# Performance work log

Hardware: AMD Instinct MI355X
Metric: run time of the kernel (lower is better)

The kernel has to match this reference:

```python
import jax, jax.numpy as jnp
import numpy as np

B = 16384          # batch_size / n_samples
SRC = 200          # source_num
C = 10             # category_size
I = SRC * C        # input_size = 2000
EPS = 1e-10


def setup_inputs() -> dict:
    key = jax.random.key(0)
    ks = jax.random.split(key, 8)
    # forward data
    x = jax.random.uniform(ks[0], (B, I), dtype=jnp.float32)
    mask = jax.random.uniform(ks[1], (B, I), dtype=jnp.float32)
    y_target = jax.random.uniform(ks[2], (B, C), dtype=jnp.float32)
    # learned parameters (xavier-uniform style init)
    def xavier(k, shape):
        fan_in, fan_out = shape[0], shape[1]
        limit = float(np.sqrt(2.0)) * float(np.sqrt(6.0 / (fan_in + fan_out)))
        return jax.random.uniform(k, shape, dtype=jnp.float32, minval=-limit, maxval=limit)
    W_reconstr = xavier(ks[3], (C, I))
    b_reconstr = xavier(ks[4], (1, I))
    W_yc = xavier(ks[5], (I, C))
    b_yc = xavier(ks[6], (1, C))
    return {"x": x, "mask": mask, "y_target": y_target,
            "W_reconstr": W_reconstr, "b_reconstr": b_reconstr,
            "W_yc": W_yc, "b_yc": b_yc}


def reference(x, mask, y_target, W_reconstr, b_reconstr, W_yc, b_yc):
    # ---- decoder (collapsed): constant_y[i] is a batch of identical one-hot
    # rows at category i, so y @ W_reconstr + b == W_reconstr[i] + b for all
    # batch elements. Stack over all i -> logits [C, I].
    logits = W_reconstr + b_reconstr                      # [C, I]
    e = jnp.exp(logits).reshape(C, SRC, C)                # per-source blocks
    # block-diagonal matmul == segmented sum over each source's C entries
    p = (e / e.sum(axis=-1, keepdims=True)).reshape(C, I)  # [C, I]
    logp = jnp.log(EPS + p)                               # [C, I]
    # -mean_j(mask * x * log p_i) per category i -> [B, C]
    reconstr_x = -(x * mask) @ logp.T / I

    # ---- encoder
    y_classifier = jax.nn.softmax(x @ W_yc + b_yc, axis=1)  # [B, C]

    # ---- losses
    loss_w_l1 = jnp.sum(jnp.abs(W_yc))
    loss_classifier_y_x = jnp.mean(jnp.sum(y_classifier * reconstr_x, axis=1))
    loss_y_kl = jnp.mean(jnp.sum(
        y_classifier * (jnp.log(EPS + y_classifier) - jnp.log(EPS + y_target)),
        axis=1))
    loss = (loss_classifier_y_x + 1e-4 * loss_y_kl
            + 0.005 / SRC / C / C * loss_w_l1)
    return (y_classifier, loss)
```

## Files before the change

### kernel.cpp

```cpp
#include <hip/hip_runtime.h>
#include <hip/hip_bf16.h>

#define B_SZ 16384
#define SRCN 200
#define CAT  10
#define IN   2000
#define QCOL 500
#define QPAD 512
#define NCHQ 8
#define TQB  10240
#define LDS_BUF0 20480
#define EPSF 1e-10f

typedef float f32x4 __attribute__((ext_vector_type(4)));
typedef _Float16 half2v __attribute__((ext_vector_type(2)));

#if __has_builtin(__builtin_amdgcn_fdot2)
__device__ __forceinline__ float fdot2(half2v a, half2v b, float c) {
    return __builtin_amdgcn_fdot2(a, b, c, false);
}
#else
__device__ __forceinline__ float fdot2(half2v a, half2v b, float c) {
    return c + (float)a[0] * (float)b[0] + (float)a[1] * (float)b[1];
}
#endif

__device__ __forceinline__ half2v pkrtz(float a, float b) {
#if __has_builtin(__builtin_amdgcn_cvt_pkrtz)
    union { __fp16 __attribute__((ext_vector_type(2))) i; half2v o; } v;
    v.i = __builtin_amdgcn_cvt_pkrtz(a, b);
    return v.o;
#else
    half2v r; r[0] = (_Float16)a; r[1] = (_Float16)b; return r;
#endif
}

__device__ __forceinline__ half2v as_h2(unsigned u) {
    union { unsigned u; half2v h; } v; v.u = u; return v.h;
}

__device__ __forceinline__ short f2h(float f) {
    union { _Float16 h; short s; } v; v.h = (_Float16)f; return v.s;
}

__device__ __forceinline__ void gload16(const void* g, void* l) {
    __builtin_amdgcn_global_load_lds(
        (const __attribute__((address_space(1))) void*)g,
        (__attribute__((address_space(3))) void*)l,
        16, 0, 0);
}

__global__ void prep_kernel(const float* __restrict__ W_rec,
                            const float* __restrict__ b_rec,
                            const float* __restrict__ W_yc,
                            short* __restrict__ lp4,
                            short* __restrict__ wy4,
                            double* __restrict__ acc) {
    if (blockIdx.x == gridDim.x - 1) {
        float p = 0.f;
        for (int i = threadIdx.x; i < IN * CAT; i += blockDim.x) p += fabsf(W_yc[i]);
        __shared__ float red[4];
        for (int o = 32; o; o >>= 1) p += __shfl_down(p, o, 64);
        if ((threadIdx.x & 63) == 0) red[threadIdx.x >> 6] = p;
        __syncthreads();
        if (threadIdx.x == 0) {
            acc[0] = 0.0; acc[1] = 0.0;
            acc[2] = (double)(red[0] + red[1] + red[2] + red[3]);
        }
        return;
    }
    int idx = blockIdx.x * blockDim.x + threadIdx.x;
    int q   = idx / (CAT * QPAD);
    int rem = idx % (CAT * QPAD);
    int n   = rem >> 9;
    int kk  = rem & 511;
    short wv = 0, lv = 0;
    if (kk < QCOL) {
        int k = q * QCOL + kk;
        wv = f2h(W_yc[k * CAT + n]);
        int base = (k / CAT) * CAT;
        float lg[CAT];
        float m = -1e30f;
        #pragma unroll
        for (int i = 0; i < CAT; i++) {
            lg[i] = W_rec[n * IN + base + i] + b_rec[base + i];
            m = fmaxf(m, lg[i]);
        }
        float s = 0.f;
        #pragma unroll
        for (int i = 0; i < CAT; i++) s += expf(lg[i] - m);
        float myl = W_rec[n * IN + k] + b_rec[k];
        float pp = expf(myl - m) / s;
        lv = f2h(logf(EPSF + pp));
    }
    lp4[idx] = lv;
    wy4[idx] = wv;
}

__global__ __launch_bounds__(512, 3) void main_kernel(
        const float* __restrict__ x, const float* __restrict__ mask,
        const short* __restrict__ lp4, const short* __restrict__ wy4,
        float* __restrict__ part) {
    __shared__ __attribute__((aligned(16))) char lds[LDS_BUF0 + 8 * 4096];

    const int tid = threadIdx.x;
    {
        const int q = blockIdx.x & 3;
        const uint4* s1 = (const uint4*)(lp4 + q * (CAT * QPAD));
        const uint4* s2 = (const uint4*)(wy4 + q * (CAT * QPAD));
        uint4* d1 = (uint4*)lds;
        uint4* d2 = (uint4*)(lds + TQB);
        #pragma unroll
        for (int i = 0; i < 2; ++i) {
            int j = i * 512 + tid;
            if (j < 640) { d1[j] = s1[j]; d2[j] = s2[j]; }
        }
    }
    __syncthreads();

    const int l  = tid & 63;
    const int w  = tid >> 6;
    const int g  = l >> 4;
    const int li = l & 15;
    const int rt = blockIdx.x >> 2;
    const int q  = blockIdx.x & 3;
    const int row = rt * 32 + w * 4 + g;

    const float* xrow = x + (size_t)row * IN;
    const float* mrow = mask + (size_t)row * IN;
    const int colb = q * QCOL + li * 4;
    char* buf = lds + LDS_BUF0 + w * 4096;

    float pR[CAT], pW[CAT];
    #pragma unroll
    for (int c = 0; c < CAT; ++c) { pR[c] = 0.f; pW[c] = 0.f; }

    auto stage = [&](int cc) {
        int col = colb + cc * 64;
        if (col > IN - 4) col = IN - 4;
        char* slot = buf + (cc & 1) * 2048;
        gload16(xrow + col, slot);
        gload16(mrow + col, slot + 1024);
    };

    auto compute = [&](int cc) {
        char* slot = buf + (cc & 1) * 2048;
        const int myo = g * 256 + li * 16;
        f32x4 xv = *(const f32x4*)(slot + myo);
        f32x4 mv = *(const f32x4*)(slot + 1024 + myo);
        half2v ax0 = pkrtz(xv[0], xv[1]);
        half2v ax1 = pkrtz(xv[2], xv[3]);
        half2v am0 = pkrtz(xv[0] * mv[0], xv[1] * mv[1]);
        half2v am1 = pkrtz(xv[2] * mv[2], xv[3] * mv[3]);
        const int tb = cc * 128 + li * 8;
        #pragma unroll
        for (int c = 0; c < CAT; ++c) {
            const uint2 lpv = *(const uint2*)(lds + c * 1024 + tb);
            const uint2 wyv = *(const uint2*)(lds + TQB + c * 1024 + tb);
            pR[c] = fdot2(am0, as_h2(lpv.x), pR[c]);
            pR[c] = fdot2(am1, as_h2(lpv.y), pR[c]);
            pW[c] = fdot2(ax0, as_h2(wyv.x), pW[c]);
            pW[c] = fdot2(ax1, as_h2(wyv.y), pW[c]);
        }
    };

    stage(0);
    stage(1);
    #pragma unroll
    for (int cc = 0; cc < NCHQ; ++cc) {
        if (cc < NCHQ - 1) { asm volatile("s_waitcnt vmcnt(2)" ::: "memory"); }
        else               { asm volatile("s_waitcnt vmcnt(0)" ::: "memory"); }
        compute(cc);
        asm volatile("s_waitcnt lgkmcnt(0)" ::: "memory");
        if (cc + 2 < NCHQ) stage(cc + 2);
    }

    #pragma unroll
    for (int c = 0; c < CAT; ++c) {
        #pragma unroll
        for (int o = 1; o < 16; o <<= 1) {
            pR[c] += __shfl_xor(pR[c], o, 64);
            pW[c] += __shfl_xor(pW[c], o, 64);
        }
    }
    if (li == 0) {
        float* pp = part + ((size_t)row * 4 + q) * 20;
        #pragma unroll
        for (int c = 0; c < CAT; ++c) { pp[c] = pR[c]; pp[10 + c] = pW[c]; }
    }
}

__global__ void combine_kernel(const float* __restrict__ part,
                               const float* __restrict__ y_target,
                               const float* __restrict__ b_yc,
                               float* __restrict__ out,
                               double* __restrict__ acc) {
    const int row = blockIdx.x * 256 + threadIdx.x;
    const float* pp = part + (size_t)row * 80;
    float pR[CAT], pW[CAT];
    #pragma unroll
    for (int c = 0; c < CAT; ++c) {
        pR[c] = pp[c] + pp[20 + c] + pp[40 + c] + pp[60 + c];
        pW[c] = pp[10 + c] + pp[30 + c] + pp[50 + c] + pp[70 + c] + b_yc[c];
    }
    float mx = -1e30f;
    #pragma unroll
    for (int c = 0; c < CAT; ++c) mx = fmaxf(mx, pW[c]);
    float y[CAT], s = 0.f;
    #pragma unroll
    for (int c = 0; c < CAT; ++c) { y[c] = __expf(pW[c] - mx); s += y[c]; }
    const float is = 1.f / s;
    float cls = 0.f, kl = 0.f;
    float* op = out + (size_t)row * CAT;
    #pragma unroll
    for (int c = 0; c < CAT; ++c) {
        y[c] *= is;
        op[c] = y[c];
        cls += y[c] * (-pR[c] * (1.f / IN));
        const float yt = y_target[(size_t)row * CAT + c];
        kl += y[c] * (__logf(EPSF + y[c]) - __logf(EPSF + yt));
    }
    #pragma unroll
    for (int o = 32; o; o >>= 1) {
        cls += __shfl_down(cls, o, 64);
        kl  += __shfl_down(kl, o, 64);
    }
    __shared__ float rc[4], rk[4];
    if ((threadIdx.x & 63) == 0) {
        rc[threadIdx.x >> 6] = cls; rk[threadIdx.x >> 6] = kl;
    }
    __syncthreads();
    if (threadIdx.x == 0) {
        atomicAdd(&acc[0], (double)(rc[0] + rc[1] + rc[2] + rc[3]));
        atomicAdd(&acc[1], (double)(rk[0] + rk[1] + rk[2] + rk[3]));
    }
}

__global__ void final_kernel(const double* __restrict__ acc,
                             float* __restrict__ out) {
    if (threadIdx.x == 0) {
        double loss = acc[0] / (double)B_SZ
                    + 1e-4 * (acc[1] / (double)B_SZ)
                    + (0.005 / (double)SRCN / (double)CAT / (double)CAT) * acc[2];
        out[(size_t)B_SZ * CAT] = (float)loss;
    }
}

extern "C" void kernel_launch(void* const* d_in, const int* in_sizes, int n_in,
                              void* d_out, int out_size, void* d_ws, size_t ws_size,
                              hipStream_t stream) {
    const float* x        = (const float*)d_in[0];
    const float* mask     = (const float*)d_in[1];
    const float* y_target = (const float*)d_in[2];
    const float* W_rec    = (const float*)d_in[3];
    const float* b_rec    = (const float*)d_in[4];
    const float* W_yc     = (const float*)d_in[5];
    const float* b_yc     = (const float*)d_in[6];
    float* out  = (float*)d_out;
    double* acc = (double*)d_ws;
    short* lp4  = (short*)((char*)d_ws + 256);
    short* wy4  = lp4 + 4 * CAT * QPAD;
    float* part = (float*)((char*)d_ws + 256 + 2 * 40960);

    prep_kernel<<<81, 256, 0, stream>>>(W_rec, b_rec, W_yc, lp4, wy4, acc);
    main_kernel<<<2048, 512, 0, stream>>>(x, mask, lp4, wy4, part);
    combine_kernel<<<64, 256, 0, stream>>>(part, y_target, b_yc, out, acc);
    final_kernel<<<1, 64, 0, stream>>>(acc, out);
}
```

Before: 79.79 us.

## Replace LDS-staged double-buffered loads with direct register loads of all chunks

The main kernel stops staging x and mask chunks through LDS with global_load_lds and manual waitcnt double buffering. Each thread now issues all eight float4 loads of x and mask into registers up front, then computes. Blocks shrink from 512 to 256 threads, covering 16 rows instead of 32, and the grid doubles to keep total work the same. This exposes more memory-level parallelism per thread and drops the LDS round trip, at the cost of higher register pressure and smaller blocks that each re-copy the lookup tables into LDS.

```diff
diff --git a/kernel.cpp b/kernel.cpp
--- a/kernel.cpp
+++ b/kernel.cpp
@@ -7,12 +7,9 @@
 #define IN   2000
 #define QCOL 500
 #define QPAD 512
-#define NCHQ 8
 #define TQB  10240
-#define LDS_BUF0 20480
 #define EPSF 1e-10f
 
-typedef float f32x4 __attribute__((ext_vector_type(4)));
 typedef _Float16 half2v __attribute__((ext_vector_type(2)));
 
 #if __has_builtin(__builtin_amdgcn_fdot2)
@@ -41,13 +38,6 @@
 
 __device__ __forceinline__ short f2h(float f) {
     union { _Float16 h; short s; } v; v.h = (_Float16)f; return v.s;
-}
-
-__device__ __forceinline__ void gload16(const void* g, void* l) {
-    __builtin_amdgcn_global_load_lds(
-        (const __attribute__((address_space(1))) void*)g,
-        (__attribute__((address_space(3))) void*)l,
-        16, 0, 0);
 }
 
 __global__ void prep_kernel(const float* __restrict__ W_rec,
@@ -97,61 +87,59 @@
     wy4[idx] = wv;
 }
 
-__global__ __launch_bounds__(512, 3) void main_kernel(
+__global__ __launch_bounds__(256, 4) void main_kernel(
         const float* __restrict__ x, const float* __restrict__ mask,
         const short* __restrict__ lp4, const short* __restrict__ wy4,
         float* __restrict__ part) {
-    __shared__ __attribute__((aligned(16))) char lds[LDS_BUF0 + 8 * 4096];
-
-    const int tid = threadIdx.x;
+    __shared__ __attribute__((aligned(16))) char lds[2 * TQB];
+
+    const int q = blockIdx.x & 3;
     {
-        const int q = blockIdx.x & 3;
         const uint4* s1 = (const uint4*)(lp4 + q * (CAT * QPAD));
         const uint4* s2 = (const uint4*)(wy4 + q * (CAT * QPAD));
         uint4* d1 = (uint4*)lds;
         uint4* d2 = (uint4*)(lds + TQB);
         #pragma unroll
-        for (int i = 0; i < 2; ++i) {
-            int j = i * 512 + tid;
+        for (int i = 0; i < 3; ++i) {
+            int j = i * 256 + threadIdx.x;
             if (j < 640) { d1[j] = s1[j]; d2[j] = s2[j]; }
         }
     }
     __syncthreads();
 
-    const int l  = tid & 63;
-    const int w  = tid >> 6;
+    const int l  = threadIdx.x & 63;
+    const int w  = threadIdx.x >> 6;
     const int g  = l >> 4;
     const int li = l & 15;
-    const int rt = blockIdx.x >> 2;
-    const int q  = blockIdx.x & 3;
-    const int row = rt * 32 + w * 4 + g;
-
-    const float* xrow = x + (size_t)row * IN;
-    const float* mrow = mask + (size_t)row * IN;
-    const int colb = q * QCOL + li * 4;
-    char* buf = lds + LDS_BUF0 + w * 4096;
+    const int row = (blockIdx.x >> 2) * 16 + w * 4 + g;
+
+    const int col0 = q * QCOL + li * 4;
+    const float* xr = x + (size_t)row * IN + col0;
+    const float* mr = mask + (size_t)row * IN + col0;
+
+    float4 xv[8], mv[8];
+    #pragma unroll
+    for (int cc = 0; cc < 7; ++cc) {
+        xv[cc] = *(const float4*)(xr + cc * 64);
+        mv[cc] = *(const float4*)(mr + cc * 64);
+    }
+    {
+        const int base = col0 + 7 * 64;
+        const int adj = (base > IN - 4) ? (base - (IN - 4)) : 0;
+        xv[7] = *(const float4*)(xr + 7 * 64 - adj);
+        mv[7] = *(const float4*)(mr + 7 * 64 - adj);
+    }
 
     float pR[CAT], pW[CAT];
     #pragma unroll
     for (int c = 0; c < CAT; ++c) { pR[c] = 0.f; pW[c] = 0.f; }
 
-    auto stage = [&](int cc) {
-        int col = colb + cc * 64;
-        if (col > IN - 4) col = IN - 4;
-        char* slot = buf + (cc & 1) * 2048;
-        gload16(xrow + col, slot);
-        gload16(mrow + col, slot + 1024);
-    };
-
-    auto compute = [&](int cc) {
-        char* slot = buf + (cc & 1) * 2048;
-        const int myo = g * 256 + li * 16;
-        f32x4 xv = *(const f32x4*)(slot + myo);
-        f32x4 mv = *(const f32x4*)(slot + 1024 + myo);
-        half2v ax0 = pkrtz(xv[0], xv[1]);
-        half2v ax1 = pkrtz(xv[2], xv[3]);
-        half2v am0 = pkrtz(xv[0] * mv[0], xv[1] * mv[1]);
-        half2v am1 = pkrtz(xv[2] * mv[2], xv[3] * mv[3]);
+    #pragma unroll
+    for (int cc = 0; cc < 8; ++cc) {
+        const half2v ax0 = pkrtz(xv[cc].x, xv[cc].y);
+        const half2v ax1 = pkrtz(xv[cc].z, xv[cc].w);
+        const half2v am0 = pkrtz(xv[cc].x * mv[cc].x, xv[cc].y * mv[cc].y);
+        const half2v am1 = pkrtz(xv[cc].z * mv[cc].z, xv[cc].w * mv[cc].w);
         const int tb = cc * 128 + li * 8;
         #pragma unroll
         for (int c = 0; c < CAT; ++c) {
@@ -162,17 +150,6 @@
             pW[c] = fdot2(ax0, as_h2(wyv.x), pW[c]);
             pW[c] = fdot2(ax1, as_h2(wyv.y), pW[c]);
         }
-    };
-
-    stage(0);
-    stage(1);
-    #pragma unroll
-    for (int cc = 0; cc < NCHQ; ++cc) {
-        if (cc < NCHQ - 1) { asm volatile("s_waitcnt vmcnt(2)" ::: "memory"); }
-        else               { asm volatile("s_waitcnt vmcnt(0)" ::: "memory"); }
-        compute(cc);
-        asm volatile("s_waitcnt lgkmcnt(0)" ::: "memory");
-        if (cc + 2 < NCHQ) stage(cc + 2);
     }
 
     #pragma unroll
@@ -263,7 +240,7 @@
     float* part = (float*)((char*)d_ws + 256 + 2 * 40960);
 
     prep_kernel<<<81, 256, 0, stream>>>(W_rec, b_rec, W_yc, lp4, wy4, acc);
-    main_kernel<<<2048, 512, 0, stream>>>(x, mask, lp4, wy4, part);
+    main_kernel<<<4096, 256, 0, stream>>>(x, mask, lp4, wy4, part);
     combine_kernel<<<64, 256, 0, stream>>>(part, y_target, b_yc, out, acc);
     final_kernel<<<1, 64, 0, stream>>>(acc, out);
 }
```

Result: faster. 72.99 us (-8.5%).
